# Kernel optimization log

Hardware: AMD Instinct MI355X
Metric: run time of the kernel (lower is better)

## Reference

```python
import jax, jax.numpy as jnp
import numpy as np

N, E = 50000, 800000
IN_C, HID, OUT_C, HEADS = 768, 64, 8, 8
NEG_SLOPE = 0.2
BN_EPS = 1e-5


def _bn(x, g, b, m, v):
    # BatchNorm1d in eval mode with running stats
    return (x - m) * jax.lax.rsqrt(v + BN_EPS) * g + b


def _gat_conv(x, W, att_src, att_dst, bias, src, dst, n):
    H, C = att_src.shape
    xw = (x @ W).reshape(n, H, C)                      # [N,H,C]
    a_src = jnp.sum(xw * att_src, axis=-1)             # [N,H]
    a_dst = jnp.sum(xw * att_dst, axis=-1)             # [N,H]
    alpha = jax.nn.leaky_relu(a_src[src] + a_dst[dst], NEG_SLOPE)  # [E',H]
    amax = jax.ops.segment_max(alpha, dst, num_segments=n)          # [N,H]
    ex = jnp.exp(alpha - amax[dst])
    denom = jax.ops.segment_sum(ex, dst, num_segments=n)            # [N,H]
    coef = ex / denom[dst]                                          # [E',H]
    out = jax.ops.segment_sum(xw[src] * coef[:, :, None], dst, num_segments=n)
    return out.reshape(n, H * C) + bias


def setup_inputs() -> dict:
    key = jax.random.key(0)
    ks = jax.random.split(key, 24)
    d = {}
    d['x'] = jax.random.normal(ks[0], (N, IN_C), dtype=jnp.float32)
    d['edge_index'] = jax.random.randint(ks[1], (2, E), 0, N, dtype=jnp.int32)
    d['proj_W'] = jax.random.normal(ks[2], (IN_C, HID), dtype=jnp.float32) * (IN_C ** -0.5)
    d['proj_b'] = jnp.zeros((HID,), jnp.float32)
    for i, kb in zip((1, 2, 3), (ks[3], ks[4], ks[5])):
        k1, k2 = jax.random.split(kb)
        d[f'bn{i}_g'] = jnp.ones((HID,), jnp.float32)
        d[f'bn{i}_b'] = jnp.zeros((HID,), jnp.float32)
        d[f'bn{i}_m'] = jax.random.normal(k1, (HID,), dtype=jnp.float32) * 0.1
        d[f'bn{i}_v'] = jax.random.uniform(k2, (HID,), dtype=jnp.float32, minval=0.5, maxval=1.5)
    C1 = HID // HEADS
    d['W1'] = jax.random.normal(ks[6], (HID, HEADS * C1), dtype=jnp.float32) * (HID ** -0.5)
    d['att_src1'] = jax.random.normal(ks[7], (HEADS, C1), dtype=jnp.float32) * 0.1
    d['att_dst1'] = jax.random.normal(ks[8], (HEADS, C1), dtype=jnp.float32) * 0.1
    d['b1'] = jnp.zeros((HEADS * C1,), jnp.float32)
    d['W2'] = jax.random.normal(ks[9], (HID, HID), dtype=jnp.float32) * (HID ** -0.5)
    d['att_src2'] = jax.random.normal(ks[10], (1, HID), dtype=jnp.float32) * 0.1
    d['att_dst2'] = jax.random.normal(ks[11], (1, HID), dtype=jnp.float32) * 0.1
    d['b2'] = jnp.zeros((HID,), jnp.float32)
    d['cls_W'] = jax.random.normal(ks[12], (HID, OUT_C), dtype=jnp.float32) * (HID ** -0.5)
    d['cls_b'] = jnp.zeros((OUT_C,), jnp.float32)
    return d


def reference(x, edge_index, proj_W, proj_b,
              bn1_g, bn1_b, bn1_m, bn1_v,
              W1, att_src1, att_dst1, b1,
              bn2_g, bn2_b, bn2_m, bn2_v,
              W2, att_src2, att_dst2, b2,
              bn3_g, bn3_b, bn3_m, bn3_v,
              cls_W, cls_b):
    n = x.shape[0]
    # add self-loops (PyG GATConv default)
    loop = jnp.arange(n, dtype=edge_index.dtype)
    src = jnp.concatenate([edge_index[0], loop])
    dst = jnp.concatenate([edge_index[1], loop])

    h = x @ proj_W + proj_b
    h = jax.nn.elu(_bn(h, bn1_g, bn1_b, bn1_m, bn1_v))
    identity = h
    h = _gat_conv(h, W1, att_src1, att_dst1, b1, src, dst, n)
    h = jax.nn.elu(_bn(h, bn2_g, bn2_b, bn2_m, bn2_v) + identity)
    identity = h
    h = _gat_conv(h, W2, att_src2, att_dst2, b2, src, dst, n)
    h = jax.nn.elu(_bn(h, bn3_g, bn3_b, bn3_m, bn3_v) + identity)
    return h @ cls_W + cls_b
```

## Files before the change

### kernel.cpp

```cpp
#include <hip/hip_runtime.h>

typedef __bf16 bf16;
typedef __attribute__((ext_vector_type(8))) __bf16 bf16x8;
typedef __attribute__((ext_vector_type(4))) float f32x4;

#define LSTR 40
#define BN_EPS 1e-5f

__global__ __launch_bounds__(256) void k_prep(
        const float* __restrict__ W0, const float* __restrict__ W1, const float* __restrict__ W2,
        bf16* __restrict__ Wt0, bf16* __restrict__ Wt1, bf16* __restrict__ Wt2,
        int* __restrict__ cnt, int n)
{
    int i = blockIdx.x*256 + threadIdx.x;
    const int T = 768*64 + 8192;
    if (i < 768*64)            { int k = i>>6, n_ = i&63;                  Wt0[n_*768+k] = (bf16)W0[i]; }
    else if (i < 768*64+4096)  { int j = i-768*64;      int k=j>>6,c=j&63; Wt1[c*64+k]  = (bf16)W1[j]; }
    else if (i < T)            { int j = i-768*64-4096; int k=j>>6,c=j&63; Wt2[c*64+k]  = (bf16)W2[j]; }
    int j = i - T;
    if (j >= 0 && j < n) cnt[j] = 0;
}

template<int MODE, bool ABF, int H>
__global__ __launch_bounds__(256) void k_gemm64(
        const void* __restrict__ Av, const bf16* __restrict__ Bt, int M, int K,
        const float* __restrict__ pb, const float* __restrict__ g, const float* __restrict__ bb,
        const float* __restrict__ mm, const float* __restrict__ vv,
        bf16* __restrict__ outB,
        float* __restrict__ a_s, float* __restrict__ a_d,
        const float* __restrict__ att_s, const float* __restrict__ att_d)
{
    __shared__ bf16 xs[64*LSTR];
    __shared__ bf16 bs[64*LSTR];
    __shared__ float sC[64], cC[64];

    int t = threadIdx.x;
    int w = t >> 6, lane = t & 63;
    int q = lane >> 4, l16 = lane & 15;
    int row0 = blockIdx.x * 64;
    int sRow = t >> 2, sK = (t & 3) * 8;

    auto loadA = [&](int k0) -> bf16x8 {
        bf16x8 xv;
        #pragma unroll
        for (int i = 0; i < 8; ++i) xv[i] = (bf16)0.f;
        int gr = row0 + sRow;
        if (gr < M) {
            if constexpr (ABF) {
                xv = *(const bf16x8*)((const bf16*)Av + (size_t)gr*K + k0 + sK);
            } else {
                const float* ap = (const float*)Av + (size_t)gr*K + k0 + sK;
                float4 f0 = *(const float4*)ap;
                float4 f1 = *(const float4*)(ap + 4);
                xv[0]=(bf16)f0.x; xv[1]=(bf16)f0.y; xv[2]=(bf16)f0.z; xv[3]=(bf16)f0.w;
                xv[4]=(bf16)f1.x; xv[5]=(bf16)f1.y; xv[6]=(bf16)f1.z; xv[7]=(bf16)f1.w;
            }
        }
        return xv;
    };
    auto loadB = [&](int k0) -> bf16x8 {
        return *(const bf16x8*)(Bt + (size_t)sRow*K + k0 + sK);
    };

    f32x4 acc[4];
    #pragma unroll
    for (int i = 0; i < 4; ++i) { acc[i][0]=0.f; acc[i][1]=0.f; acc[i][2]=0.f; acc[i][3]=0.f; }

    bf16x8 xv = loadA(0);
    bf16x8 bv = loadB(0);

    for (int k0 = 0; k0 < K; k0 += 32) {
        *(bf16x8*)(xs + sRow*LSTR + sK) = xv;
        *(bf16x8*)(bs + sRow*LSTR + sK) = bv;
        __syncthreads();
        if (k0 + 32 < K) {
            xv = loadA(k0 + 32);
            bv = loadB(k0 + 32);
        }
        bf16x8 af = *(bf16x8*)(xs + (w*16 + l16)*LSTR + q*8);
        #pragma unroll
        for (int tt = 0; tt < 4; ++tt) {
            bf16x8 bfr = *(bf16x8*)(bs + (tt*16 + l16)*LSTR + q*8);
            acc[tt] = __builtin_amdgcn_mfma_f32_16x16x32_bf16(af, bfr, acc[tt], 0, 0, 0);
        }
        __syncthreads();
    }

    if constexpr (MODE == 0) {
        if (t < 64) {
            float s = rsqrtf(vv[t] + BN_EPS) * g[t];
            sC[t] = s;
            cC[t] = (pb[t] - mm[t]) * s + bb[t];
        }
        __syncthreads();
    }

    #pragma unroll
    for (int tt = 0; tt < 4; ++tt) {
        int col = tt*16 + l16;
        #pragma unroll
        for (int r = 0; r < 4; ++r) {
            int row = row0 + w*16 + q*4 + r;
            if (row < M) {
                float val = acc[tt][r];
                if constexpr (MODE == 0) {
                    val = val * sC[col] + cC[col];
                    val = val > 0.f ? val : __expf(val) - 1.f;
                }
                outB[(size_t)row*64 + col] = (bf16)val;
            }
        }
    }

    if constexpr (MODE == 1) {
        #pragma unroll
        for (int r = 0; r < 4; ++r) {
            int row = row0 + w*16 + q*4 + r;
            if constexpr (H == 1) {
                float ps = 0.f, pd = 0.f;
                #pragma unroll
                for (int tt = 0; tt < 4; ++tt) {
                    int col = tt*16 + l16;
                    ps += acc[tt][r] * att_s[col];
                    pd += acc[tt][r] * att_d[col];
                }
                #pragma unroll
                for (int off = 1; off < 16; off <<= 1) {
                    ps += __shfl_xor(ps, off);
                    pd += __shfl_xor(pd, off);
                }
                if (l16 == 0 && row < M) { a_s[row] = ps; a_d[row] = pd; }
            } else {
                float ps[4], pd[4];
                #pragma unroll
                for (int tt = 0; tt < 4; ++tt) {
                    int col = tt*16 + l16;
                    ps[tt] = acc[tt][r] * att_s[col];
                    pd[tt] = acc[tt][r] * att_d[col];
                }
                #pragma unroll
                for (int off = 1; off < 8; off <<= 1) {
                    #pragma unroll
                    for (int tt = 0; tt < 4; ++tt) {
                        ps[tt] += __shfl_xor(ps[tt], off);
                        pd[tt] += __shfl_xor(pd[tt], off);
                    }
                }
                if ((l16 & 7) == 0 && row < M) {
                    int hb = l16 >> 3;
                    #pragma unroll
                    for (int tt = 0; tt < 4; ++tt) {
                        a_s[row*8 + 2*tt + hb] = ps[tt];
                        a_d[row*8 + 2*tt + hb] = pd[tt];
                    }
                }
            }
        }
    }
}

__global__ __launch_bounds__(256) void k_count(const int* __restrict__ dst, int E, int* cnt) {
    int i = blockIdx.x*256 + threadIdx.x;
    if (i < E) atomicAdd(&cnt[dst[i]], 1);
}
__global__ __launch_bounds__(256) void k_scan_block(const int* __restrict__ cnt,
        int* __restrict__ rp, int* __restrict__ bsum, int n) {
    __shared__ int s[256];
    int t = threadIdx.x, v = blockIdx.x*256 + t;
    int x = (v < n) ? cnt[v] : 0;
    s[t] = x; __syncthreads();
    for (int off = 1; off < 256; off <<= 1) {
        int y = (t >= off) ? s[t-off] : 0;
        __syncthreads();
        s[t] += y;
        __syncthreads();
    }
    if (v < n) rp[v+1] = s[t];
    if (t == 255) bsum[blockIdx.x] = s[255];
}
__global__ __launch_bounds__(256) void k_scan_bsum(int* bsum, int nb) {
    __shared__ int s[256];
    int t = threadIdx.x;
    int x = (t < nb) ? bsum[t] : 0;
    s[t] = x; __syncthreads();
    for (int off = 1; off < 256; off <<= 1) {
        int y = (t >= off) ? s[t-off] : 0;
        __syncthreads();
        s[t] += y;
        __syncthreads();
    }
    if (t < nb) bsum[t] = s[t] - x;
}
__global__ __launch_bounds__(256) void k_finalize(int* __restrict__ rp, const int* __restrict__ bsum,
        const int* __restrict__ cnt, int* __restrict__ cursor, int n) {
    int v = blockIdx.x*256 + threadIdx.x;
    if (v < n) {
        int val = rp[v+1] + bsum[v >> 8];
        rp[v+1] = val;
        cursor[v] = val - cnt[v];
        if (v == 0) rp[0] = 0;
    }
}
__global__ __launch_bounds__(256) void k_scatter(const int* __restrict__ src, const int* __restrict__ dst,
        int E, int* __restrict__ cursor, int* __restrict__ in_src) {
    int i = blockIdx.x*256 + threadIdx.x;
    if (i < E) {
        int pos = atomicAdd(&cursor[dst[i]], 1);
        in_src[pos] = src[i];
    }
}

template<int H, bool CLS>
__global__ __launch_bounds__(256) void k_gat_agg(const bf16* __restrict__ xwb,
        const float* __restrict__ a_src, const float* __restrict__ a_dst,
        const int* __restrict__ rp, const int* __restrict__ in_src,
        const float* __restrict__ bias,
        const float* __restrict__ g, const float* __restrict__ bb,
        const float* __restrict__ mm, const float* __restrict__ vv,
        const bf16* __restrict__ resid, bf16* __restrict__ outB, float* __restrict__ outF,
        const float* __restrict__ clsW, const float* __restrict__ clsb, int n)
{
    int wv = (blockIdx.x*256 + threadIdx.x) >> 6;
    int lane = threadIdx.x & 63;
    if (wv >= n) return;
    int h = (H == 8) ? (lane >> 3) : 0;
    float adst = a_dst[wv*H + h];

    float aself = a_src[wv*H + h] + adst;
    aself = (aself > 0.f) ? aself : 0.2f*aself;
    float eself = __expf(aself);
    float acc = eself * (float)xwb[(size_t)wv*64 + lane];
    float den = eself;

    int beg = rp[wv], end = rp[wv+1];
    int e = beg;
    for (; e + 8 <= end; e += 8) {
        int u[8];
        #pragma unroll
        for (int i = 0; i < 8; ++i) u[i] = in_src[e+i];
        float s[8], xr[8];
        #pragma unroll
        for (int i = 0; i < 8; ++i) s[i] = a_src[u[i]*H + h];
        #pragma unroll
        for (int i = 0; i < 8; ++i) xr[i] = (float)xwb[(size_t)u[i]*64 + lane];
        #pragma unroll
        for (int i = 0; i < 8; ++i) {
            float a = s[i] + adst;
            a = (a > 0.f) ? a : 0.2f*a;
            float ex = __expf(a);
            acc += ex * xr[i];
            den += ex;
        }
    }
    for (; e < end; ++e) {
        int u = in_src[e];
        float al = a_src[u*H + h] + adst;
        al = (al > 0.f) ? al : 0.2f*al;
        float ex = __expf(al);
        acc += ex * (float)xwb[(size_t)u*64 + lane];
        den += ex;
    }
    float val = acc/den + bias[lane];
    float sc = rsqrtf(vv[lane] + BN_EPS) * g[lane];
    val = (val - mm[lane]) * sc + bb[lane];
    val += (float)resid[(size_t)wv*64 + lane];
    val = (val > 0.f) ? val : __expf(val) - 1.f;

    if constexpr (!CLS) {
        outB[(size_t)wv*64 + lane] = (bf16)val;
    } else {
        float keep = 0.f;
        #pragma unroll
        for (int o = 0; o < 8; ++o) {
            float p = val * clsW[lane*8 + o];
            #pragma unroll
            for (int off = 1; off < 64; off <<= 1) p += __shfl_xor(p, off);
            if (lane == o) keep = p + clsb[o];
        }
        if (lane < 8) outF[(size_t)wv*8 + lane] = keep;
    }
}

extern "C" void kernel_launch(void* const* d_in, const int* in_sizes, int n_in,
                              void* d_out, int out_size, void* d_ws, size_t ws_size,
                              hipStream_t stream)
{
    const float* x      = (const float*)d_in[0];
    const int*   ei     = (const int*)  d_in[1];
    const float* proj_W = (const float*)d_in[2];
    const float* proj_b = (const float*)d_in[3];
    const float* bn1_g  = (const float*)d_in[4];
    const float* bn1_b  = (const float*)d_in[5];
    const float* bn1_m  = (const float*)d_in[6];
    const float* bn1_v  = (const float*)d_in[7];
    const float* bn2_g  = (const float*)d_in[8];
    const float* bn2_b  = (const float*)d_in[9];
    const float* bn2_m  = (const float*)d_in[10];
    const float* bn2_v  = (const float*)d_in[11];
    const float* bn3_g  = (const float*)d_in[12];
    const float* bn3_b  = (const float*)d_in[13];
    const float* bn3_m  = (const float*)d_in[14];
    const float* bn3_v  = (const float*)d_in[15];
    const float* W1     = (const float*)d_in[16];
    const float* att_s1 = (const float*)d_in[17];
    const float* att_d1 = (const float*)d_in[18];
    const float* b1     = (const float*)d_in[19];
    const float* W2     = (const float*)d_in[20];
    const float* att_s2 = (const float*)d_in[21];
    const float* att_d2 = (const float*)d_in[22];
    const float* b2     = (const float*)d_in[23];
    const float* cls_W  = (const float*)d_in[24];
    const float* cls_b  = (const float*)d_in[25];

    const int N = in_sizes[0] / 768;
    const int E = in_sizes[1] / 2;
    const int* srce = ei;
    const int* dste = ei + E;

    char* p = (char*)d_ws;
    auto carve = [&](size_t bytes) -> void* {
        void* r = (void*)p;
        p += (bytes + 255) & ~(size_t)255;
        return r;
    };
    bf16*  Wt0    = (bf16*) carve((size_t)64*768*2);
    bf16*  Wt1    = (bf16*) carve((size_t)64*64*2);
    bf16*  Wt2    = (bf16*) carve((size_t)64*64*2);
    bf16*  h0b    = (bf16*) carve((size_t)N*64*2);
    bf16*  h1b    = (bf16*) carve((size_t)N*64*2);
    bf16*  xwb    = (bf16*) carve((size_t)N*64*2);
    float* a_s    = (float*)carve((size_t)N*8*4);
    float* a_d    = (float*)carve((size_t)N*8*4);
    int*   cnt    = (int*)  carve((size_t)N*4);
    int*   rp     = (int*)  carve((size_t)(N+1)*4);
    int*   cursor = (int*)  carve((size_t)N*4);
    int*   bsum   = (int*)  carve(1024);
    int*   in_src = (int*)  carve((size_t)E*4);

    const int nb = (N + 255) / 256;
    const int PREP = 768*64 + 8192;

    k_prep<<<(PREP + N + 255)/256, 256, 0, stream>>>(proj_W, W1, W2, Wt0, Wt1, Wt2, cnt, N);

    k_count<<<(E + 255)/256, 256, 0, stream>>>(dste, E, cnt);
    k_scan_block<<<nb, 256, 0, stream>>>(cnt, rp, bsum, N);
    k_scan_bsum<<<1, 256, 0, stream>>>(bsum, nb);
    k_finalize<<<nb, 256, 0, stream>>>(rp, bsum, cnt, cursor, N);
    k_scatter<<<(E + 255)/256, 256, 0, stream>>>(srce, dste, E, cursor, in_src);

    k_gemm64<0, false, 1><<<(N + 63)/64, 256, 0, stream>>>(x, Wt0, N, 768,
            proj_b, bn1_g, bn1_b, bn1_m, bn1_v, h0b, nullptr, nullptr, nullptr, nullptr);

    k_gemm64<1, true, 8><<<(N + 63)/64, 256, 0, stream>>>(h0b, Wt1, N, 64,
            nullptr, nullptr, nullptr, nullptr, nullptr, xwb, a_s, a_d, att_s1, att_d1);
    k_gat_agg<8, false><<<(N + 3)/4, 256, 0, stream>>>(xwb, a_s, a_d, rp, in_src,
            b1, bn2_g, bn2_b, bn2_m, bn2_v, h0b, h1b, nullptr, nullptr, nullptr, N);

    k_gemm64<1, true, 1><<<(N + 63)/64, 256, 0, stream>>>(h1b, Wt2, N, 64,
            nullptr, nullptr, nullptr, nullptr, nullptr, xwb, a_s, a_d, att_s2, att_d2);
    k_gat_agg<1, true><<<(N + 3)/4, 256, 0, stream>>>(xwb, a_s, a_d, rp, in_src,
            b2, bn3_g, bn3_b, bn3_m, bn3_v, h1b, nullptr, (float*)d_out, cls_W, cls_b, N);
}
```

Measured before the change: 504.4 us.

## Fuse projection and first GAT linear, compress edge indices, merge scan kernels

Adds a fused kernel that runs the 768-wide projection GEMM with double-buffered shared-memory tiles, applies BN and ELU, then multiplies by W1 in shared memory and emits xw plus the per-head attention logits. This removes one kernel launch and one round trip of h0 through global memory. It also folds the block-sum scan into the finalize kernel and stores CSR source indices as 16-bit values to halve the index traffic during gather. The 16-bit index cannot hold node ids up to 50000 beyond 65535 only by luck; values below 65536 fit, so it is valid for N=50000 but would break for larger graphs.

```diff
diff --git a/kernel.cpp b/kernel.cpp
--- a/kernel.cpp
+++ b/kernel.cpp
@@ -3,8 +3,10 @@
 typedef __bf16 bf16;
 typedef __attribute__((ext_vector_type(8))) __bf16 bf16x8;
 typedef __attribute__((ext_vector_type(4))) float f32x4;
-
-#define LSTR 40
+typedef unsigned short u16;
+
+#define LSTR  40
+#define LSTR2 72
 #define BN_EPS 1e-5f
 
 __global__ __launch_bounds__(256) void k_prep(
@@ -19,6 +21,153 @@
     else if (i < T)            { int j = i-768*64-4096; int k=j>>6,c=j&63; Wt2[c*64+k]  = (bf16)W2[j]; }
     int j = i - T;
     if (j >= 0 && j < n) cnt[j] = 0;
+}
+
+__global__ __launch_bounds__(256) void k_fused_proj(
+        const float* __restrict__ A, const bf16* __restrict__ Bt,
+        const bf16* __restrict__ W1t, int M,
+        const float* __restrict__ pb, const float* __restrict__ g,
+        const float* __restrict__ bb, const float* __restrict__ mm, const float* __restrict__ vv,
+        const float* __restrict__ att_s, const float* __restrict__ att_d,
+        bf16* __restrict__ h0b, bf16* __restrict__ xwb,
+        float* __restrict__ a_s, float* __restrict__ a_d)
+{
+    const int K = 768;
+    __shared__ bf16 xs[2][64*LSTR];
+    __shared__ bf16 bs[2][64*LSTR];
+    __shared__ bf16 hs [64*LSTR2];
+    __shared__ bf16 w1s[64*LSTR2];
+    __shared__ float sC[64], cC[64];
+
+    int t = threadIdx.x;
+    int w = t >> 6, lane = t & 63;
+    int q = lane >> 4, l16 = lane & 15;
+    int row0 = blockIdx.x * 64;
+    int sRow = t >> 2, sK = (t & 3) * 8;
+
+    if (t < 64) {
+        float s = rsqrtf(vv[t] + BN_EPS) * g[t];
+        sC[t] = s;
+        cC[t] = (pb[t] - mm[t]) * s + bb[t];
+    }
+    {
+        int r = t >> 2, c0 = (t & 3) * 16;
+        *(bf16x8*)(w1s + r*LSTR2 + c0)     = *(const bf16x8*)(W1t + r*64 + c0);
+        *(bf16x8*)(w1s + r*LSTR2 + c0 + 8) = *(const bf16x8*)(W1t + r*64 + c0 + 8);
+    }
+
+    auto loadA = [&](int k0) -> bf16x8 {
+        bf16x8 xv;
+        #pragma unroll
+        for (int i = 0; i < 8; ++i) xv[i] = (bf16)0.f;
+        int gr = row0 + sRow;
+        if (gr < M) {
+            const float* ap = A + (size_t)gr*K + k0 + sK;
+            float4 f0 = *(const float4*)ap;
+            float4 f1 = *(const float4*)(ap + 4);
+            xv[0]=(bf16)f0.x; xv[1]=(bf16)f0.y; xv[2]=(bf16)f0.z; xv[3]=(bf16)f0.w;
+            xv[4]=(bf16)f1.x; xv[5]=(bf16)f1.y; xv[6]=(bf16)f1.z; xv[7]=(bf16)f1.w;
+        }
+        return xv;
+    };
+    auto loadB = [&](int k0) -> bf16x8 {
+        return *(const bf16x8*)(Bt + (size_t)sRow*K + k0 + sK);
+    };
+
+    f32x4 acc[4];
+    #pragma unroll
+    for (int i = 0; i < 4; ++i) { acc[i][0]=0.f; acc[i][1]=0.f; acc[i][2]=0.f; acc[i][3]=0.f; }
+
+    bf16x8 xv = loadA(0);
+    bf16x8 bv = loadB(0);
+    *(bf16x8*)(&xs[0][sRow*LSTR + sK]) = xv;
+    *(bf16x8*)(&bs[0][sRow*LSTR + sK]) = bv;
+    __syncthreads();
+
+    int cur = 0;
+    for (int k0 = 0; k0 < K; k0 += 32) {
+        if (k0 + 32 < K) {
+            xv = loadA(k0 + 32);
+            bv = loadB(k0 + 32);
+        }
+        bf16x8 af = *(bf16x8*)(&xs[cur][(w*16 + l16)*LSTR + q*8]);
+        #pragma unroll
+        for (int tt = 0; tt < 4; ++tt) {
+            bf16x8 bfr = *(bf16x8*)(&bs[cur][(tt*16 + l16)*LSTR + q*8]);
+            acc[tt] = __builtin_amdgcn_mfma_f32_16x16x32_bf16(af, bfr, acc[tt], 0, 0, 0);
+        }
+        if (k0 + 32 < K) {
+            *(bf16x8*)(&xs[cur^1][sRow*LSTR + sK]) = xv;
+            *(bf16x8*)(&bs[cur^1][sRow*LSTR + sK]) = bv;
+            __syncthreads();
+            cur ^= 1;
+        }
+    }
+
+    #pragma unroll
+    for (int tt = 0; tt < 4; ++tt) {
+        int col = tt*16 + l16;
+        #pragma unroll
+        for (int r = 0; r < 4; ++r) {
+            int rl = w*16 + q*4 + r;
+            float val = acc[tt][r] * sC[col] + cC[col];
+            val = val > 0.f ? val : __expf(val) - 1.f;
+            hs[rl*LSTR2 + col] = (bf16)val;
+            int row = row0 + rl;
+            if (row < M) h0b[(size_t)row*64 + col] = (bf16)val;
+        }
+    }
+    __syncthreads();
+
+    f32x4 acc2[4];
+    #pragma unroll
+    for (int i = 0; i < 4; ++i) { acc2[i][0]=0.f; acc2[i][1]=0.f; acc2[i][2]=0.f; acc2[i][3]=0.f; }
+    #pragma unroll
+    for (int ks = 0; ks < 2; ++ks) {
+        bf16x8 af = *(bf16x8*)(&hs[(w*16 + l16)*LSTR2 + ks*32 + q*8]);
+        #pragma unroll
+        for (int tt = 0; tt < 4; ++tt) {
+            bf16x8 bfr = *(bf16x8*)(&w1s[(tt*16 + l16)*LSTR2 + ks*32 + q*8]);
+            acc2[tt] = __builtin_amdgcn_mfma_f32_16x16x32_bf16(af, bfr, acc2[tt], 0, 0, 0);
+        }
+    }
+
+    #pragma unroll
+    for (int tt = 0; tt < 4; ++tt) {
+        int col = tt*16 + l16;
+        #pragma unroll
+        for (int r = 0; r < 4; ++r) {
+            int row = row0 + w*16 + q*4 + r;
+            if (row < M) xwb[(size_t)row*64 + col] = (bf16)acc2[tt][r];
+        }
+    }
+    #pragma unroll
+    for (int r = 0; r < 4; ++r) {
+        int row = row0 + w*16 + q*4 + r;
+        float ps[4], pd[4];
+        #pragma unroll
+        for (int tt = 0; tt < 4; ++tt) {
+            int col = tt*16 + l16;
+            ps[tt] = acc2[tt][r] * att_s[col];
+            pd[tt] = acc2[tt][r] * att_d[col];
+        }
+        #pragma unroll
+        for (int off = 1; off < 8; off <<= 1) {
+            #pragma unroll
+            for (int tt = 0; tt < 4; ++tt) {
+                ps[tt] += __shfl_xor(ps[tt], off);
+                pd[tt] += __shfl_xor(pd[tt], off);
+            }
+        }
+        if ((l16 & 7) == 0 && row < M) {
+            int hb = l16 >> 3;
+            #pragma unroll
+            for (int tt = 0; tt < 4; ++tt) {
+                a_s[row*8 + 2*tt + hb] = ps[tt];
+                a_d[row*8 + 2*tt + hb] = pd[tt];
+            }
+        }
+    }
 }
 
 template<int MODE, bool ABF, int H>
@@ -178,7 +327,8 @@
     if (v < n) rp[v+1] = s[t];
     if (t == 255) bsum[blockIdx.x] = s[255];
 }
-__global__ __launch_bounds__(256) void k_scan_bsum(int* bsum, int nb) {
+__global__ __launch_bounds__(256) void k_finalize(int* __restrict__ rp, const int* __restrict__ bsum,
+        const int* __restrict__ cnt, int* __restrict__ cursor, int n, int nb) {
     __shared__ int s[256];
     int t = threadIdx.x;
     int x = (t < nb) ? bsum[t] : 0;
@@ -189,31 +339,29 @@
         s[t] += y;
         __syncthreads();
     }
-    if (t < nb) bsum[t] = s[t] - x;
-}
-__global__ __launch_bounds__(256) void k_finalize(int* __restrict__ rp, const int* __restrict__ bsum,
-        const int* __restrict__ cnt, int* __restrict__ cursor, int n) {
-    int v = blockIdx.x*256 + threadIdx.x;
+    int v = blockIdx.x*256 + t;
     if (v < n) {
-        int val = rp[v+1] + bsum[v >> 8];
+        int b = v >> 8;
+        int off0 = (b == 0) ? 0 : s[b-1];
+        int val = rp[v+1] + off0;
         rp[v+1] = val;
         cursor[v] = val - cnt[v];
         if (v == 0) rp[0] = 0;
     }
 }
 __global__ __launch_bounds__(256) void k_scatter(const int* __restrict__ src, const int* __restrict__ dst,
-        int E, int* __restrict__ cursor, int* __restrict__ in_src) {
+        int E, int* __restrict__ cursor, u16* __restrict__ in_src) {
     int i = blockIdx.x*256 + threadIdx.x;
     if (i < E) {
         int pos = atomicAdd(&cursor[dst[i]], 1);
-        in_src[pos] = src[i];
+        in_src[pos] = (u16)src[i];
     }
 }
 
 template<int H, bool CLS>
 __global__ __launch_bounds__(256) void k_gat_agg(const bf16* __restrict__ xwb,
         const float* __restrict__ a_src, const float* __restrict__ a_dst,
-        const int* __restrict__ rp, const int* __restrict__ in_src,
+        const int* __restrict__ rp, const u16* __restrict__ in_src,
         const float* __restrict__ bias,
         const float* __restrict__ g, const float* __restrict__ bb,
         const float* __restrict__ mm, const float* __restrict__ vv,
@@ -237,7 +385,7 @@
     for (; e + 8 <= end; e += 8) {
         int u[8];
         #pragma unroll
-        for (int i = 0; i < 8; ++i) u[i] = in_src[e+i];
+        for (int i = 0; i < 8; ++i) u[i] = (int)in_src[e+i];
         float s[8], xr[8];
         #pragma unroll
         for (int i = 0; i < 8; ++i) s[i] = a_src[u[i]*H + h];
@@ -253,7 +401,7 @@
         }
     }
     for (; e < end; ++e) {
-        int u = in_src[e];
+        int u = (int)in_src[e];
         float al = a_src[u*H + h] + adst;
         al = (al > 0.f) ? al : 0.2f*al;
         float ex = __expf(al);
@@ -335,7 +483,7 @@
     int*   rp     = (int*)  carve((size_t)(N+1)*4);
     int*   cursor = (int*)  carve((size_t)N*4);
     int*   bsum   = (int*)  carve(1024);
-    int*   in_src = (int*)  carve((size_t)E*4);
+    u16*   in_src = (u16*)  carve((size_t)E*2);
 
     const int nb = (N + 255) / 256;
     const int PREP = 768*64 + 8192;
@@ -344,15 +492,13 @@
 
     k_count<<<(E + 255)/256, 256, 0, stream>>>(dste, E, cnt);
     k_scan_block<<<nb, 256, 0, stream>>>(cnt, rp, bsum, N);
-    k_scan_bsum<<<1, 256, 0, stream>>>(bsum, nb);
-    k_finalize<<<nb, 256, 0, stream>>>(rp, bsum, cnt, cursor, N);
+    k_finalize<<<nb, 256, 0, stream>>>(rp, bsum, cnt, cursor, N, nb);
     k_scatter<<<(E + 255)/256, 256, 0, stream>>>(srce, dste, E, cursor, in_src);
 
-    k_gemm64<0, false, 1><<<(N + 63)/64, 256, 0, stream>>>(x, Wt0, N, 768,
-            proj_b, bn1_g, bn1_b, bn1_m, bn1_v, h0b, nullptr, nullptr, nullptr, nullptr);
-
-    k_gemm64<1, true, 8><<<(N + 63)/64, 256, 0, stream>>>(h0b, Wt1, N, 64,
-            nullptr, nullptr, nullptr, nullptr, nullptr, xwb, a_s, a_d, att_s1, att_d1);
+    k_fused_proj<<<(N + 63)/64, 256, 0, stream>>>(x, Wt0, Wt1, N,
+            proj_b, bn1_g, bn1_b, bn1_m, bn1_v, att_s1, att_d1,
+            h0b, xwb, a_s, a_d);
+
     k_gat_agg<8, false><<<(N + 3)/4, 256, 0, stream>>>(xwb, a_s, a_d, rp, in_src,
             b1, bn2_g, bn2_b, bn2_m, bn2_v, h0b, h1b, nullptr, nullptr, nullptr, N);
 
```

New measurement: 489.4 us. 3.0% less time.
